# Kernel tuning notes

Hardware: AMD Instinct MI355X
Metric: run time of the kernel (lower is better)

Reference implementation:

```python
import jax, jax.numpy as jnp
import numpy as np

BLOCK = 16
NVFP4_LEVELS = jnp.array([0.0, 0.5, 1.0, 1.5, 2.0, 3.0, 4.0, 6.0], dtype=jnp.float32)


def _quantize_to_nvfp4(x_blocks):
    # x_blocks: [n_blocks, BLOCK]
    amax = jnp.clip(jnp.max(jnp.abs(x_blocks), axis=-1, keepdims=True), 1e-12, None)
    scale = amax / 6.0
    x_norm = jnp.abs(x_blocks) / scale
    idx = jnp.argmin(jnp.abs(x_norm[..., None] - NVFP4_LEVELS), axis=-1)
    return jnp.sign(x_blocks) * NVFP4_LEVELS[idx] * scale


def setup_inputs() -> dict:
    key = jax.random.key(0)
    k1, k2, k3, k4 = jax.random.split(key, 4)
    B, S, H, O = 16, 1024, 1152, 4608
    x = jax.random.normal(k1, (B, S, H), dtype=jnp.float32)
    w_quantized = jax.random.normal(k2, (O, H), dtype=jnp.float32) * 0.02
    smooth_scale = jax.random.uniform(k3, (H,), dtype=jnp.float32, minval=0.5, maxval=2.0)
    bias = jax.random.normal(k4, (O,), dtype=jnp.float32) * 0.02
    return {"x": x, "w_quantized": w_quantized, "smooth_scale": smooth_scale, "bias": bias}


def reference(x, w_quantized, smooth_scale, bias):
    orig_shape = x.shape
    H = orig_shape[-1]
    # SmoothQuant activation prescale
    x_s = (x * smooth_scale).reshape(-1, H)              # [T, H]
    # per-token prescale to [-6, 6]
    token_max = jnp.clip(jnp.max(jnp.abs(x_s), axis=-1, keepdims=True), 1e-12, None)
    pre_scale = token_max / 6.0
    x_pre = x_s / pre_scale
    # blockwise NVFP4 fake quant
    x_q = _quantize_to_nvfp4(x_pre.reshape(-1, BLOCK)).reshape(x_s.shape)
    x_q = x_q * pre_scale                                # restore token scale
    out = x_q.reshape(orig_shape) @ w_quantized.T + bias  # F.linear
    return out
```

## Files before the change

kernel.cpp:

```cpp
#include <hip/hip_runtime.h>
#include <hip/hip_bf16.h>

typedef __attribute__((ext_vector_type(8))) _Float16 f16x8;
typedef __attribute__((ext_vector_type(4))) float  f32x4;

#define H_DIM 1152
#define H_VEC (H_DIM / 4)

__device__ __forceinline__ float nvfp4_level(float xn) {
    return xn <= 0.25f ? 0.0f
         : xn <= 0.75f ? 0.5f
         : xn <= 1.25f ? 1.0f
         : xn <= 1.75f ? 1.5f
         : xn <= 2.5f  ? 2.0f
         : xn <= 3.5f  ? 3.0f
         : xn <= 5.0f  ? 4.0f : 6.0f;
}

__global__ __launch_bounds__(256) void quant_kernel(
    const float4* __restrict__ x4, const float4* __restrict__ s4,
    _Float16* __restrict__ xq)
{
    const int t    = (blockIdx.x << 2) + (threadIdx.x >> 6);
    const int lane = threadIdx.x & 63;
    const float4* xrow = x4 + (size_t)t * H_VEC;

    float4 v[5];
    int    fidx[5];
    float  m = 0.f;
    #pragma unroll
    for (int i = 0; i < 5; ++i) {
        const int f = (i < 4) ? (lane + 64 * i) : (256 + (lane & 31));
        fidx[i] = f;
        const float4 xx = xrow[f];
        const float4 ss = s4[f];
        float4 vv;
        vv.x = xx.x * ss.x; vv.y = xx.y * ss.y;
        vv.z = xx.z * ss.z; vv.w = xx.w * ss.w;
        v[i] = vv;
        m = fmaxf(m, fmaxf(fmaxf(fabsf(vv.x), fabsf(vv.y)),
                           fmaxf(fabsf(vv.z), fabsf(vv.w))));
    }
    #pragma unroll
    for (int off = 32; off; off >>= 1)
        m = fmaxf(m, __shfl_xor(m, off, 64));
    const float pre_scale = fmaxf(m, 1e-12f) / 6.0f;

    #pragma unroll
    for (int i = 0; i < 5; ++i) {
        float4 p;
        p.x = v[i].x / pre_scale;
        p.y = v[i].y / pre_scale;
        p.z = v[i].z / pre_scale;
        p.w = v[i].w / pre_scale;
        float g = fmaxf(fmaxf(fabsf(p.x), fabsf(p.y)),
                        fmaxf(fabsf(p.z), fabsf(p.w)));
        g = fmaxf(g, __shfl_xor(g, 1, 64));
        g = fmaxf(g, __shfl_xor(g, 2, 64));
        const float scale = fmaxf(g, 1e-12f) / 6.0f;

        alignas(8) _Float16 o[4];
        {
            float q;
            q = copysignf(nvfp4_level(fabsf(p.x) / scale) * scale, p.x) * pre_scale;
            o[0] = (_Float16)q;
            q = copysignf(nvfp4_level(fabsf(p.y) / scale) * scale, p.y) * pre_scale;
            o[1] = (_Float16)q;
            q = copysignf(nvfp4_level(fabsf(p.z) / scale) * scale, p.z) * pre_scale;
            o[2] = (_Float16)q;
            q = copysignf(nvfp4_level(fabsf(p.w) / scale) * scale, p.w) * pre_scale;
            o[3] = (_Float16)q;
        }
        if (i < 4 || lane < 32) {
            _Float16* dst = xq + (size_t)t * H_DIM + fidx[i] * 4;
            *(uint2*)dst = *(const uint2*)o;
        }
    }
}

__global__ __launch_bounds__(256) void wconv_kernel(
    const float* __restrict__ w, _Float16* __restrict__ wq, int n)
{
    int i = (blockIdx.x * 256 + threadIdx.x) * 4;
    if (i < n) {
        float4 v = *(const float4*)(w + i);
        alignas(8) _Float16 o[4];
        o[0] = (_Float16)v.x;
        o[1] = (_Float16)v.y;
        o[2] = (_Float16)v.z;
        o[3] = (_Float16)v.w;
        *(uint2*)(wq + i) = *(const uint2*)o;
    }
}

__device__ __forceinline__ void async_copy16(const void* gptr, void* lptr)
{
    __builtin_amdgcn_global_load_lds(
        (const __attribute__((address_space(1))) unsigned int*)gptr,
        (__attribute__((address_space(3))) unsigned int*)lptr,
        16, 0, 0);
}

#define BARRIER() do { asm volatile("" ::: "memory"); \
                       __builtin_amdgcn_s_barrier();  \
                       asm volatile("" ::: "memory"); } while (0)

#define BM 256
#define BN 256
#define BK 64

__global__ __launch_bounds__(512, 2) void gemm_bt_kernel(
    const _Float16* __restrict__ A,
    const _Float16* __restrict__ B,
    const float* __restrict__ bias,
    float* __restrict__ C,
    int M, int N, int K)
{
    __shared__ alignas(16) _Float16 sA[2][BM * BK];
    __shared__ alignas(16) _Float16 sB[2][BN * BK];

    const int tid    = threadIdx.x;
    const int wave   = tid >> 6;
    const int lane   = tid & 63;
    const int lane16 = lane & 15;
    const int quad   = lane >> 4;

    const int nbx = gridDim.x;
    const int nwg = nbx * gridDim.y;
    int bid = blockIdx.y * nbx + blockIdx.x;
    if ((nwg & 7) == 0) {
        const int cpx = nwg >> 3;
        bid = (bid & 7) * cpx + (bid >> 3);
    }
    const int m0 = (bid / nbx) * BM;
    const int n0 = (bid % nbx) * BN;

    const int wr = wave >> 2;
    const int wc = wave & 3;

    const int NT = K / BK;

    int srcA[4], srcB[4], ldst[4];
    #pragma unroll
    for (int s = 0; s < 4; ++s) {
        const int base = (wave * 4 + s) * 64;
        const int c    = base + lane;
        const int r    = c >> 3;
        const int sw   = ((c & 7) * 8) ^ ((r & 7) << 3);
        srcA[s] = (m0 + r) * K + sw;
        srcB[s] = (n0 + r) * K + sw;
        ldst[s] = base * 16;
    }

    auto stage = [&](int t, int d) {
        const int k0 = t * BK;
        #pragma unroll
        for (int s = 0; s < 4; ++s) {
            async_copy16(A + srcA[s] + k0, (char*)(&sA[d][0]) + ldst[s]);
            async_copy16(B + srcB[s] + k0, (char*)(&sB[d][0]) + ldst[s]);
        }
    };

    stage(0, 0);
    if (NT > 1) stage(1, 1);
    asm volatile("s_waitcnt vmcnt(8)" ::: "memory");
    BARRIER();

    f32x4 acc[8][4] = {};
    f16x8 b[4][2];

    for (int t = 0; t < NT; ++t) {
        const int d = t & 1;
        const _Float16* tA = &sA[d][0];
        const _Float16* tB = &sB[d][0];

        #pragma unroll
        for (int p = 0; p < 4; ++p) {
            f16x8 a[2][2];
            #pragma unroll
            for (int ii = 0; ii < 2; ++ii) {
                const int r = wr * 128 + (p * 2 + ii) * 16 + lane16;
                #pragma unroll
                for (int ks = 0; ks < 2; ++ks)
                    a[ii][ks] = *(const f16x8*)(tA + r * 64 +
                                 ((ks * 32 + quad * 8) ^ ((r & 7) << 3)));
            }
            if (p == 0) {
                #pragma unroll
                for (int j = 0; j < 4; ++j) {
                    const int rb = wc * 64 + j * 16 + lane16;
                    #pragma unroll
                    for (int ks = 0; ks < 2; ++ks)
                        b[j][ks] = *(const f16x8*)(tB + rb * 64 +
                                    ((ks * 32 + quad * 8) ^ ((rb & 7) << 3)));
                }
            }
            BARRIER();
            asm volatile("s_waitcnt lgkmcnt(0)" ::: "memory");
            __builtin_amdgcn_s_setprio(1);
            #pragma unroll
            for (int ii = 0; ii < 2; ++ii)
                #pragma unroll
                for (int j = 0; j < 4; ++j)
                    #pragma unroll
                    for (int ks = 0; ks < 2; ++ks)
                        acc[p * 2 + ii][j] = __builtin_amdgcn_mfma_f32_16x16x32_f16(
                            a[ii][ks], b[j][ks], acc[p * 2 + ii][j], 0, 0, 0);
            __builtin_amdgcn_s_setprio(0);
            BARRIER();
        }

        if (t + 2 < NT) {
            stage(t + 2, d);
            asm volatile("s_waitcnt vmcnt(8)" ::: "memory");
        } else {
            asm volatile("s_waitcnt vmcnt(0)" ::: "memory");
        }
        BARRIER();
    }

    #pragma unroll
    for (int i = 0; i < 8; ++i) {
        const int m = m0 + wr * 128 + i * 16 + quad * 4;
        #pragma unroll
        for (int j = 0; j < 4; ++j) {
            const int n = n0 + wc * 64 + j * 16 + lane16;
            const float bv = bias[n];
            float* cp = C + (size_t)m * N + n;
            #pragma unroll
            for (int r2 = 0; r2 < 4; ++r2)
                cp[(size_t)r2 * N] = acc[i][j][r2] + bv;
        }
    }
}

extern "C" void kernel_launch(void* const* d_in, const int* in_sizes, int n_in,
                              void* d_out, int out_size, void* d_ws, size_t ws_size,
                              hipStream_t stream)
{
    const float* x      = (const float*)d_in[0];
    const float* w      = (const float*)d_in[1];
    const float* smooth = (const float*)d_in[2];
    const float* bias   = (const float*)d_in[3];
    float* out = (float*)d_out;

    const int H = in_sizes[2];
    const int T = in_sizes[0] / H;
    const int O = in_sizes[3];

    _Float16* xq = (_Float16*)d_ws;
    _Float16* wq = (_Float16*)((char*)d_ws + (size_t)T * H * sizeof(_Float16));

    quant_kernel<<<T / 4, 256, 0, stream>>>((const float4*)x, (const float4*)smooth, xq);
    wconv_kernel<<<(O * H / 4 + 255) / 256, 256, 0, stream>>>(w, wq, O * H);

    dim3 grid(O / BN, T / BM);
    gemm_bt_kernel<<<grid, 512, 0, stream>>>(xq, wq, bias, out, T, O, H);
}
```

Baseline: 576.3 us.

## Double-buffer A fragments from LDS and issue next-tile prefetch before final MFMA phase

```diff
diff --git a/kernel.cpp b/kernel.cpp
--- a/kernel.cpp
+++ b/kernel.cpp
@@ -101,10 +101,6 @@
         16, 0, 0);
 }
 
-#define BARRIER() do { asm volatile("" ::: "memory"); \
-                       __builtin_amdgcn_s_barrier();  \
-                       asm volatile("" ::: "memory"); } while (0)
-
 #define BM 256
 #define BN 256
 #define BK 64
@@ -137,7 +133,6 @@
 
     const int wr = wave >> 2;
     const int wc = wave & 3;
-
     const int NT = K / BK;
 
     int srcA[4], srcB[4], ldst[4];
@@ -161,42 +156,58 @@
         }
     };
 
+    const int xr = (lane16 & 7) << 3;
+
     stage(0, 0);
     if (NT > 1) stage(1, 1);
     asm volatile("s_waitcnt vmcnt(8)" ::: "memory");
-    BARRIER();
+    __builtin_amdgcn_s_barrier();
+    asm volatile("" ::: "memory");
 
     f32x4 acc[8][4] = {};
-    f16x8 b[4][2];
 
     for (int t = 0; t < NT; ++t) {
         const int d = t & 1;
         const _Float16* tA = &sA[d][0];
         const _Float16* tB = &sB[d][0];
 
+        f16x8 b[4][2];
+        f16x8 a[2][2][2];
+
+        #pragma unroll
+        for (int j = 0; j < 4; ++j) {
+            const int rb = wc * 64 + j * 16 + lane16;
+            #pragma unroll
+            for (int ks = 0; ks < 2; ++ks)
+                b[j][ks] = *(const f16x8*)(tB + rb * 64 + ((ks * 32 + quad * 8) ^ xr));
+        }
+        #pragma unroll
+        for (int ii = 0; ii < 2; ++ii) {
+            const int r = wr * 128 + ii * 16 + lane16;
+            #pragma unroll
+            for (int ks = 0; ks < 2; ++ks)
+                a[0][ii][ks] = *(const f16x8*)(tA + r * 64 + ((ks * 32 + quad * 8) ^ xr));
+        }
+
         #pragma unroll
         for (int p = 0; p < 4; ++p) {
-            f16x8 a[2][2];
-            #pragma unroll
-            for (int ii = 0; ii < 2; ++ii) {
-                const int r = wr * 128 + (p * 2 + ii) * 16 + lane16;
+            if (p < 3) {
                 #pragma unroll
-                for (int ks = 0; ks < 2; ++ks)
-                    a[ii][ks] = *(const f16x8*)(tA + r * 64 +
-                                 ((ks * 32 + quad * 8) ^ ((r & 7) << 3)));
-            }
-            if (p == 0) {
-                #pragma unroll
-                for (int j = 0; j < 4; ++j) {
-                    const int rb = wc * 64 + j * 16 + lane16;
+                for (int ii = 0; ii < 2; ++ii) {
+                    const int r = wr * 128 + ((p + 1) * 2 + ii) * 16 + lane16;
                     #pragma unroll
                     for (int ks = 0; ks < 2; ++ks)
-                        b[j][ks] = *(const f16x8*)(tB + rb * 64 +
-                                    ((ks * 32 + quad * 8) ^ ((rb & 7) << 3)));
+                        a[(p + 1) & 1][ii][ks] =
+                            *(const f16x8*)(tA + r * 64 + ((ks * 32 + quad * 8) ^ xr));
                 }
+            } else {
+                asm volatile("s_waitcnt lgkmcnt(0)" ::: "memory");
             }
-            BARRIER();
-            asm volatile("s_waitcnt lgkmcnt(0)" ::: "memory");
+            __builtin_amdgcn_s_barrier();
+            if (p == 3) {
+                asm volatile("" ::: "memory");
+                if (t + 2 < NT) stage(t + 2, d);
+            }
             __builtin_amdgcn_s_setprio(1);
             #pragma unroll
             for (int ii = 0; ii < 2; ++ii)
@@ -205,18 +216,14 @@
                     #pragma unroll
                     for (int ks = 0; ks < 2; ++ks)
                         acc[p * 2 + ii][j] = __builtin_amdgcn_mfma_f32_16x16x32_f16(
-                            a[ii][ks], b[j][ks], acc[p * 2 + ii][j], 0, 0, 0);
+                            a[p & 1][ii][ks], b[j][ks], acc[p * 2 + ii][j], 0, 0, 0);
             __builtin_amdgcn_s_setprio(0);
-            BARRIER();
-        }
-
-        if (t + 2 < NT) {
-            stage(t + 2, d);
-            asm volatile("s_waitcnt vmcnt(8)" ::: "memory");
-        } else {
-            asm volatile("s_waitcnt vmcnt(0)" ::: "memory");
-        }
-        BARRIER();
+        }
+
+        if (t + 2 < NT) asm volatile("s_waitcnt vmcnt(8)" ::: "memory");
+        else            asm volatile("s_waitcnt vmcnt(0)" ::: "memory");
+        __builtin_amdgcn_s_barrier();
+        asm volatile("" ::: "memory");
     }
 
     #pragma unroll
```

New measurement: 556.9 us. 3.4% less time.
